# Kernel tuning notes

Hardware: AMD Instinct MI355X
Metric: run time of the kernel (lower is better)

## Reference

```python
import jax, jax.numpy as jnp
import numpy as np

B, S, D = 2, 2048, 1024
H = 16
HS = D // H  # head_size = 64
SCALE = HS ** 0.5


def setup_inputs() -> dict:
    key = jax.random.key(0)
    ks = jax.random.split(key, 7)
    std = 1.0 / np.sqrt(D)
    return {
        "x": jax.random.normal(ks[0], (B, S, D), dtype=jnp.float32),
        "Wq": jax.random.normal(ks[1], (D, D), dtype=jnp.float32) * std,
        "bq": jax.random.normal(ks[2], (D,), dtype=jnp.float32) * std,
        "Wk": jax.random.normal(ks[3], (D, D), dtype=jnp.float32) * std,
        "bk": jax.random.normal(ks[4], (D,), dtype=jnp.float32) * std,
        "Wv": jax.random.normal(ks[5], (D, D), dtype=jnp.float32) * std,
        "bv": jax.random.normal(ks[6], (D,), dtype=jnp.float32) * std,
    }


def reference(x, Wq, bq, Wk, bk, Wv, bv):
    bs, seq, _ = x.shape
    # QKV projections (torch Linear: x @ W.T + b)
    Q = (x @ Wq.T + bq).reshape(bs, seq, H, HS)
    K = (x @ Wk.T + bk).reshape(bs, seq, H, HS)
    V = (x @ Wv.T + bv).reshape(bs, seq, H, HS)
    # scores[b,h,q,k] = Q . K / scale
    scores = jnp.einsum("bqhd,bkhd->bhqk", Q, K) / SCALE
    # causal mask: disallow k > q
    causal = jnp.triu(jnp.ones((seq, seq), dtype=bool), k=1)
    scores = jnp.where(causal, -jnp.inf, scores)
    probs = jax.nn.softmax(scores, axis=-1)
    att = jnp.einsum("bhqk,bkhd->bqhd", probs, V)
    return att.reshape(bs, seq, H * HS)
```

## Files before the change

kernel.cpp:

```cpp
#include <hip/hip_runtime.h>

typedef unsigned short ushort_t;
typedef __bf16 bf16x8 __attribute__((ext_vector_type(8)));
typedef unsigned short ushortx8 __attribute__((ext_vector_type(8)));
typedef unsigned short ushortx4 __attribute__((ext_vector_type(4)));
typedef unsigned int uintx4 __attribute__((ext_vector_type(4)));
typedef float floatx4 __attribute__((ext_vector_type(4)));

__device__ inline void load16_lds(const ushort_t* g, ushort_t* l) {
  __builtin_amdgcn_global_load_lds(
      (__attribute__((address_space(1))) void*)(g),
      (__attribute__((address_space(3))) void*)(l),
      16, 0, 0);
}

__device__ inline float bf2f(ushort_t u) {
  unsigned int v = ((unsigned int)u) << 16;
  return __builtin_bit_cast(float, v);
}

__device__ inline ushort_t f2bf(float f) {
  unsigned int u = __builtin_bit_cast(unsigned int, f);
  u += 0x7fffu + ((u >> 16) & 1u);
  return (ushort_t)(u >> 16);
}

__device__ inline bf16x8 ldfrag(const ushort_t* p) {
  return __builtin_bit_cast(bf16x8, *(const ushortx8*)p);
}

__device__ inline bool sniff_f32(const ushort_t* x, int lane_off) {
  float v = fabsf(bf2f(x[lane_off]));
  bool big = !(v < 1e4f);
  return __ballot(big) != 0ull;
}

__global__ __launch_bounds__(256) void convert_all(
    const void* __restrict__ x,
    const void* __restrict__ wq, const void* __restrict__ wk, const void* __restrict__ wv,
    const void* __restrict__ bq, const void* __restrict__ bk, const void* __restrict__ bv,
    ushort_t* __restrict__ xb, ushort_t* __restrict__ wqb,
    ushort_t* __restrict__ wkb, ushort_t* __restrict__ wvb,
    float* __restrict__ biasf, int* __restrict__ flag)
{
  const bool f32 = sniff_f32((const ushort_t*)x, (int)(threadIdx.x & 63));
  const int seg = blockIdx.y;
  if (seg == 4) {
    if (blockIdx.x == 0 && threadIdx.x == 0) *flag = f32 ? 1 : 0;
    const int i = blockIdx.x * 256 + threadIdx.x;
    if (i >= 1024) return;
    const void* bs[3] = {bq, bk, bv};
#pragma unroll
    for (int k = 0; k < 3; ++k)
      biasf[k * 1024 + i] = f32 ? ((const float*)bs[k])[i] : bf2f(((const ushort_t*)bs[k])[i]);
    return;
  }
  const void* src = (seg == 0) ? x : (seg == 1) ? wq : (seg == 2) ? wk : wv;
  ushort_t* dst   = (seg == 0) ? xb : (seg == 1) ? wqb : (seg == 2) ? wkb : wvb;
  const int n = (seg == 0) ? 4194304 : 1048576;
  const int i = (blockIdx.x * 256 + threadIdx.x) * 8;
  if (i >= n) return;
  if (f32) {
    const float* s = (const float*)src + i;
    ushortx8 o;
#pragma unroll
    for (int j = 0; j < 8; ++j) o[j] = f2bf(s[j]);
    *(ushortx8*)(dst + i) = o;
  } else {
    *(ushortx8*)(dst + i) = *(const ushortx8*)((const ushort_t*)src + i);
  }
}

__global__ __launch_bounds__(256, 2) void qkv_gemm(
    const ushort_t* __restrict__ x,
    const ushort_t* __restrict__ Wq, const ushort_t* __restrict__ Wk,
    const ushort_t* __restrict__ Wv, const float* __restrict__ biasf,
    ushort_t* __restrict__ Qo, ushort_t* __restrict__ Ko, ushort_t* __restrict__ Vt)
{
  __shared__ __attribute__((aligned(16))) ushort_t As[128 * 32];
  __shared__ __attribute__((aligned(16))) ushort_t Bs[128 * 32];

  const int which = blockIdx.z;
  const ushort_t* W = (which == 0) ? Wq : (which == 1) ? Wk : Wv;
  const float oscale = (which == 0) ? 0.18033688011112042f : 1.0f;

  const int n0 = blockIdx.x * 128;
  const int m0 = blockIdx.y * 128;

  const int tid  = threadIdx.x;
  const int wave = tid >> 6;
  const int lane = tid & 63;
  const int ln   = lane & 15;
  const int quad = lane >> 4;
  const int wm = (wave >> 1) * 64;
  const int wn = (wave & 1) * 64;

  floatx4 acc[4][4];
#pragma unroll
  for (int i = 0; i < 4; ++i)
#pragma unroll
    for (int j = 0; j < 4; ++j) acc[i][j] = floatx4{0.f, 0.f, 0.f, 0.f};

  const int c1 = tid, c2 = tid + 256;
  const ushort_t* ga1 = x + (m0 + (c1 >> 2)) * 1024 + (c1 & 3) * 8;
  const ushort_t* ga2 = x + (m0 + (c2 >> 2)) * 1024 + (c2 & 3) * 8;
  const ushort_t* gb1 = W + (n0 + (c1 >> 2)) * 1024 + (c1 & 3) * 8;
  const ushort_t* gb2 = W + (n0 + (c2 >> 2)) * 1024 + (c2 & 3) * 8;
  ushort_t* la1 = As + wave * 512;
  ushort_t* la2 = As + 2048 + wave * 512;
  ushort_t* lb1 = Bs + wave * 512;
  ushort_t* lb2 = Bs + 2048 + wave * 512;

  for (int kt = 0; kt < 1024; kt += 32) {
    __syncthreads();
    load16_lds(ga1 + kt, la1);
    load16_lds(ga2 + kt, la2);
    load16_lds(gb1 + kt, lb1);
    load16_lds(gb2 + kt, lb2);
    __syncthreads();

    bf16x8 af[4], bfr[4];
#pragma unroll
    for (int mi = 0; mi < 4; ++mi)
      af[mi] = ldfrag(As + (wm + mi * 16 + ln) * 32 + quad * 8);
#pragma unroll
    for (int ni = 0; ni < 4; ++ni)
      bfr[ni] = ldfrag(Bs + (wn + ni * 16 + ln) * 32 + quad * 8);
#pragma unroll
    for (int mi = 0; mi < 4; ++mi)
#pragma unroll
      for (int ni = 0; ni < 4; ++ni)
        acc[mi][ni] = __builtin_amdgcn_mfma_f32_16x16x32_bf16(af[mi], bfr[ni], acc[mi][ni], 0, 0, 0);
  }

  float bvv[4];
#pragma unroll
  for (int ni = 0; ni < 4; ++ni) bvv[ni] = biasf[which * 1024 + n0 + wn + ni * 16 + ln];

  if (which == 2) {
#pragma unroll
    for (int mi = 0; mi < 4; ++mi)
#pragma unroll
      for (int ni = 0; ni < 4; ++ni) {
        const int col = n0 + wn + ni * 16 + ln;
        const int row0 = m0 + wm + mi * 16 + quad * 4;
        const int b = row0 >> 11, s0 = row0 & 2047;
        const int h = col >> 6, hs = col & 63;
        ushortx4 pk;
#pragma unroll
        for (int r = 0; r < 4; ++r) pk[r] = f2bf(acc[mi][ni][r] + bvv[ni]);
        *(ushortx4*)(Vt + ((size_t)((b * 16 + h) * 64 + hs)) * 2048 + s0) = pk;
      }
  } else {
    ushort_t* out = (which == 0) ? Qo : Ko;
#pragma unroll
    for (int mi = 0; mi < 4; ++mi)
#pragma unroll
      for (int ni = 0; ni < 4; ++ni) {
        const int col = n0 + wn + ni * 16 + ln;
#pragma unroll
        for (int r = 0; r < 4; ++r) {
          const int row = m0 + wm + mi * 16 + quad * 4 + r;
          out[row * 1024 + col] = f2bf((acc[mi][ni][r] + bvv[ni]) * oscale);
        }
      }
  }
}

__global__ __launch_bounds__(128) void flash8(
    const ushort_t* __restrict__ Q, const ushort_t* __restrict__ Kx,
    const ushort_t* __restrict__ Vt, void* __restrict__ out,
    const int* __restrict__ flag)
{
  __shared__ __attribute__((aligned(16))) float Cb[64][68];
  __shared__ float lbuf[64][4];

  const bool f32o = (*flag != 0);
  const int tid  = threadIdx.x;
  const int wave = tid >> 6;
  const int lane = tid & 63;
  const int ln = lane & 15, quad = lane >> 4;

  const int idxA = (ln + 32 * (quad & 1)) * 4;
  const int idxB = idxA + 64;
  const bool hiq = (quad >> 1) != 0;

  const int i = blockIdx.x;
  const int xcd = i & 7, j = i >> 3;
  const int bh = xcd * 4 + (j & 3);
  const int cc = 31 - (j >> 2);
  const int b = bh >> 4, h = bh & 15;
  const int qw = cc * 64;
  const int ntiles = cc + 1;

  const ushort_t* kbase = Kx + ((size_t)b * 2048) * 1024 + h * 64;
  const ushort_t* vbase = Vt + (size_t)bh * 64 * 2048;

  bf16x8 qf[4][2];
#pragma unroll
  for (int bi = 0; bi < 4; ++bi)
#pragma unroll
    for (int ks = 0; ks < 2; ++ks)
      qf[bi][ks] = ldfrag(Q + (size_t)(b * 2048 + qw + bi * 16 + ln) * 1024 + h * 64 + ks * 32 + quad * 8);

  floatx4 ot[4][4];
#pragma unroll
  for (int ai = 0; ai < 4; ++ai)
#pragma unroll
    for (int bi = 0; bi < 4; ++bi) ot[ai][bi] = floatx4{0.f, 0.f, 0.f, 0.f};
  float li[4] = {0.f, 0.f, 0.f, 0.f};

  for (int t = wave; t < ntiles; t += 2) {
    const int kv0 = t * 64;
    const bool diag = (t == ntiles - 1);

    const ushort_t* kp = kbase + (size_t)(kv0 + ln) * 1024 + quad * 8;
    bf16x8 kf[4][2];
#pragma unroll
    for (int mi = 0; mi < 4; ++mi)
#pragma unroll
      for (int ks = 0; ks < 2; ++ks)
        kf[mi][ks] = ldfrag(kp + mi * 16 * 1024 + ks * 32);

    const ushort_t* vp = vbase + (size_t)ln * 2048 + kv0 + quad * 8;
    bf16x8 vf[4][2];
#pragma unroll
    for (int ai = 0; ai < 4; ++ai)
#pragma unroll
      for (int ks = 0; ks < 2; ++ks)
        vf[ai][ks] = ldfrag(vp + ai * 16 * 2048 + ks * 32);

#pragma unroll
    for (int bi = 0; bi < 4; ++bi) {
      floatx4 st[4];
#pragma unroll
      for (int mi = 0; mi < 4; ++mi) st[mi] = floatx4{0.f, 0.f, 0.f, 0.f};
#pragma unroll
      for (int mi = 0; mi < 4; ++mi) {
        st[mi] = __builtin_amdgcn_mfma_f32_16x16x32_bf16(kf[mi][0], qf[bi][0], st[mi], 0, 0, 0);
        st[mi] = __builtin_amdgcn_mfma_f32_16x16x32_bf16(kf[mi][1], qf[bi][1], st[mi], 0, 0, 0);
      }

      const int qrow = qw + bi * 16 + ln;
      float p[4][4];
      if (diag) {
#pragma unroll
        for (int mi = 0; mi < 4; ++mi)
#pragma unroll
          for (int r = 0; r < 4; ++r) {
            const int kv = kv0 + mi * 16 + quad * 4 + r;
            const float e = __builtin_amdgcn_exp2f(st[mi][r]);
            p[mi][r] = (kv > qrow) ? 0.f : e;
          }
      } else {
#pragma unroll
        for (int mi = 0; mi < 4; ++mi)
#pragma unroll
          for (int r = 0; r < 4; ++r) p[mi][r] = __builtin_amdgcn_exp2f(st[mi][r]);
      }

      unsigned d[4][2];
#pragma unroll
      for (int mi = 0; mi < 4; ++mi) {
        li[bi] += (p[mi][0] + p[mi][1]) + (p[mi][2] + p[mi][3]);
        d[mi][0] = __builtin_amdgcn_perm(
            __builtin_bit_cast(unsigned, p[mi][1]), __builtin_bit_cast(unsigned, p[mi][0]), 0x07060302u);
        d[mi][1] = __builtin_amdgcn_perm(
            __builtin_bit_cast(unsigned, p[mi][3]), __builtin_bit_cast(unsigned, p[mi][2]), 0x07060302u);
      }

      bf16x8 pb[2];
#pragma unroll
      for (int ks = 0; ks < 2; ++ks) {
        uintx4 w;
#pragma unroll
        for (int jj = 0; jj < 4; ++jj) {
          const int idx = (jj >> 1) ? idxB : idxA;
          const int lo = __builtin_amdgcn_ds_bpermute(idx, (int)d[2 * ks][jj & 1]);
          const int hi = __builtin_amdgcn_ds_bpermute(idx, (int)d[2 * ks + 1][jj & 1]);
          w[jj] = (unsigned)(hiq ? hi : lo);
        }
        pb[ks] = __builtin_bit_cast(bf16x8, w);
      }

#pragma unroll
      for (int ai = 0; ai < 4; ++ai) {
        ot[ai][bi] = __builtin_amdgcn_mfma_f32_16x16x32_bf16(vf[ai][0], pb[0], ot[ai][bi], 0, 0, 0);
        ot[ai][bi] = __builtin_amdgcn_mfma_f32_16x16x32_bf16(vf[ai][1], pb[1], ot[ai][bi], 0, 0, 0);
      }
    }
  }

  if (wave == 1) {
#pragma unroll
    for (int bi = 0; bi < 4; ++bi) {
#pragma unroll
      for (int ai = 0; ai < 4; ++ai)
        *(floatx4*)&Cb[bi * 16 + ln][ai * 16 + quad * 4] = ot[ai][bi];
      lbuf[bi * 16 + ln][quad] = 0.f;
    }
#pragma unroll
    for (int bi = 0; bi < 4; ++bi) lbuf[lane][bi] = li[bi];
  }
  __syncthreads();
  if (wave == 0) {
#pragma unroll
    for (int bi = 0; bi < 4; ++bi) {
#pragma unroll
      for (int ai = 0; ai < 4; ++ai) {
        const floatx4 o = *(const floatx4*)&Cb[bi * 16 + ln][ai * 16 + quad * 4];
#pragma unroll
        for (int r = 0; r < 4; ++r) ot[ai][bi][r] += o[r];
      }
      li[bi] += lbuf[lane][bi];
    }

#pragma unroll
    for (int bi = 0; bi < 4; ++bi) {
      li[bi] += __shfl_xor(li[bi], 16);
      li[bi] += __shfl_xor(li[bi], 32);
      const float inv = 1.0f / li[bi];
      const int qrow = qw + bi * 16 + ln;
      if (f32o) {
        float* of = (float*)out;
#pragma unroll
        for (int ai = 0; ai < 4; ++ai) {
          floatx4 o;
#pragma unroll
          for (int r = 0; r < 4; ++r) o[r] = ot[ai][bi][r] * inv;
          *(floatx4*)(of + (size_t)(b * 2048 + qrow) * 1024 + h * 64 + ai * 16 + quad * 4) = o;
        }
      } else {
        ushort_t* ob = (ushort_t*)out;
#pragma unroll
        for (int ai = 0; ai < 4; ++ai) {
          ushortx4 pk;
#pragma unroll
          for (int r = 0; r < 4; ++r) pk[r] = f2bf(ot[ai][bi][r] * inv);
          *(ushortx4*)(ob + (size_t)(b * 2048 + qrow) * 1024 + h * 64 + ai * 16 + quad * 4) = pk;
        }
      }
    }
  }
}

extern "C" void kernel_launch(void* const* d_in, const int* in_sizes, int n_in,
                              void* d_out, int out_size, void* d_ws, size_t ws_size,
                              hipStream_t stream) {
  char* w = (char*)d_ws;
  int* flag = (int*)w;
  size_t off = 256;
  ushort_t* xb  = (ushort_t*)(w + off); off += (size_t)4194304 * 2;
  ushort_t* wqb = (ushort_t*)(w + off); off += (size_t)1048576 * 2;
  ushort_t* wkb = (ushort_t*)(w + off); off += (size_t)1048576 * 2;
  ushort_t* wvb = (ushort_t*)(w + off); off += (size_t)1048576 * 2;
  float* biasf  = (float*)(w + off);    off += (size_t)3 * 1024 * 4;
  ushort_t* Qw  = (ushort_t*)(w + off); off += (size_t)4194304 * 2;
  ushort_t* Kw  = (ushort_t*)(w + off); off += (size_t)4194304 * 2;
  ushort_t* Vtw = (ushort_t*)(w + off);

  convert_all<<<dim3(2048, 5), 256, 0, stream>>>(
      d_in[0], d_in[1], d_in[3], d_in[5], d_in[2], d_in[4], d_in[6],
      xb, wqb, wkb, wvb, biasf, flag);
  qkv_gemm<<<dim3(8, 32, 3), 256, 0, stream>>>(xb, wqb, wkb, wvb, biasf, Qw, Kw, Vtw);
  flash8<<<1024, 128, 0, stream>>>(Qw, Kw, Vtw, d_out, flag);
}
```

Before: 162.8 us.

## Split KV tiles across four waves per flash block with tree reduction

The flash attention kernel now launches 256 threads (four waves) per query block instead of two. The waves take every fourth KV tile, so each wave walks a shorter serial chain over the causal tiles. Partial outputs and row sums are merged in two LDS steps: waves 1 and 3 fold into waves 0 and 2, then wave 2 folds into wave 0. The row sum is stored in spare columns of the padded Cb buffer, which replaces the separate lbuf array. The cost is extra barriers and LDS traffic, more waves per CU competing for registers, and idle waves on blocks with few KV tiles.

```diff
diff --git a/kernel.cpp b/kernel.cpp
--- a/kernel.cpp
+++ b/kernel.cpp
@@ -167,13 +167,12 @@
   }
 }
 
-__global__ __launch_bounds__(128) void flash8(
+__global__ __launch_bounds__(256) void flash9(
     const ushort_t* __restrict__ Q, const ushort_t* __restrict__ Kx,
     const ushort_t* __restrict__ Vt, void* __restrict__ out,
     const int* __restrict__ flag)
 {
-  __shared__ __attribute__((aligned(16))) float Cb[64][68];
-  __shared__ float lbuf[64][4];
+  __shared__ __attribute__((aligned(16))) float Cb[2][64][68];
 
   const bool f32o = (*flag != 0);
   const int tid  = threadIdx.x;
@@ -210,7 +209,7 @@
     for (int bi = 0; bi < 4; ++bi) ot[ai][bi] = floatx4{0.f, 0.f, 0.f, 0.f};
   float li[4] = {0.f, 0.f, 0.f, 0.f};
 
-  for (int t = wave; t < ntiles; t += 2) {
+  for (int t = wave; t < ntiles; t += 4) {
     const int kv0 = t * 64;
     const bool diag = (t == ntiles - 1);
 
@@ -291,16 +290,39 @@
     }
   }
 
-  if (wave == 1) {
+  if (wave == 1 || wave == 3) {
+    const int bufw = (wave == 3) ? 1 : 0;
 #pragma unroll
     for (int bi = 0; bi < 4; ++bi) {
 #pragma unroll
       for (int ai = 0; ai < 4; ++ai)
-        *(floatx4*)&Cb[bi * 16 + ln][ai * 16 + quad * 4] = ot[ai][bi];
-      lbuf[bi * 16 + ln][quad] = 0.f;
-    }
-#pragma unroll
-    for (int bi = 0; bi < 4; ++bi) lbuf[lane][bi] = li[bi];
+        *(floatx4*)&Cb[bufw][bi * 16 + ln][ai * 16 + quad * 4] = ot[ai][bi];
+      Cb[bufw][bi * 16 + ln][64 + quad] = li[bi];
+    }
+  }
+  __syncthreads();
+  if (wave == 0 || wave == 2) {
+    const int bufr = (wave == 2) ? 1 : 0;
+#pragma unroll
+    for (int bi = 0; bi < 4; ++bi) {
+#pragma unroll
+      for (int ai = 0; ai < 4; ++ai) {
+        const floatx4 o = *(const floatx4*)&Cb[bufr][bi * 16 + ln][ai * 16 + quad * 4];
+#pragma unroll
+        for (int r = 0; r < 4; ++r) ot[ai][bi][r] += o[r];
+      }
+      li[bi] += Cb[bufr][bi * 16 + ln][64 + quad];
+    }
+  }
+  __syncthreads();
+  if (wave == 2) {
+#pragma unroll
+    for (int bi = 0; bi < 4; ++bi) {
+#pragma unroll
+      for (int ai = 0; ai < 4; ++ai)
+        *(floatx4*)&Cb[0][bi * 16 + ln][ai * 16 + quad * 4] = ot[ai][bi];
+      Cb[0][bi * 16 + ln][64 + quad] = li[bi];
+    }
   }
   __syncthreads();
   if (wave == 0) {
@@ -308,11 +330,11 @@
     for (int bi = 0; bi < 4; ++bi) {
 #pragma unroll
       for (int ai = 0; ai < 4; ++ai) {
-        const floatx4 o = *(const floatx4*)&Cb[bi * 16 + ln][ai * 16 + quad * 4];
+        const floatx4 o = *(const floatx4*)&Cb[0][bi * 16 + ln][ai * 16 + quad * 4];
 #pragma unroll
         for (int r = 0; r < 4; ++r) ot[ai][bi][r] += o[r];
       }
-      li[bi] += lbuf[lane][bi];
+      li[bi] += Cb[0][bi * 16 + ln][64 + quad];
     }
 
 #pragma unroll
@@ -363,5 +385,5 @@
       d_in[0], d_in[1], d_in[3], d_in[5], d_in[2], d_in[4], d_in[6],
       xb, wqb, wkb, wvb, biasf, flag);
   qkv_gemm<<<dim3(8, 32, 3), 256, 0, stream>>>(xb, wqb, wkb, wvb, biasf, Qw, Kw, Vtw);
-  flash8<<<1024, 128, 0, stream>>>(Qw, Kw, Vtw, d_out, flag);
-}
+  flash9<<<1024, 256, 0, stream>>>(Qw, Kw, Vtw, d_out, flag);
+}
```

New measurement: 174.8 us. 7.4% more time.
